# Performance work log

Hardware: AMD Instinct MI355X
Metric: run time of the kernel (lower is better)

The kernel has to match this reference:

```python
import jax, jax.numpy as jnp
import numpy as np

N_NODES = 50000
N_EDGES = 800000
IN_FEATS = 128
NUM_HEADS = 4
OUT_FEATS = 16
NEG_SLOPE = 0.2


def setup_inputs() -> dict:
    key = jax.random.key(0)
    k_feat, k_src, k_dst, k_w, k_al, k_ar = jax.random.split(key, 6)
    feat = jax.random.normal(k_feat, (N_NODES, IN_FEATS), dtype=jnp.float32)
    src = jax.random.randint(k_src, (N_EDGES,), 0, N_NODES, dtype=jnp.int32)
    # guarantee every destination node has in-degree >= 1 (segment softmax well-defined)
    dst_rand = jax.random.randint(k_dst, (N_EDGES - N_NODES,), 0, N_NODES, dtype=jnp.int32)
    dst = jnp.concatenate([jnp.arange(N_NODES, dtype=jnp.int32), dst_rand])
    # xavier-normal-ish parameter scales
    W = jax.random.normal(k_w, (IN_FEATS, NUM_HEADS * OUT_FEATS), dtype=jnp.float32) * (
        1.414 * (2.0 / (IN_FEATS + NUM_HEADS * OUT_FEATS)) ** 0.5)
    attn_l = jax.random.normal(k_al, (NUM_HEADS, OUT_FEATS), dtype=jnp.float32) * 0.1
    attn_r = jax.random.normal(k_ar, (NUM_HEADS, OUT_FEATS), dtype=jnp.float32) * 0.1
    bias = jnp.zeros((NUM_HEADS * OUT_FEATS,), dtype=jnp.float32)
    return {"feat": feat, "src": src, "dst": dst, "W": W,
            "attn_l": attn_l, "attn_r": attn_r, "bias": bias}


def reference(feat, src, dst, W, attn_l, attn_r, bias):
    N = feat.shape[0]
    H, D = attn_l.shape
    # shared projection (homogeneous-graph branch, eval mode: dropout = identity)
    ft = (feat @ W).reshape(N, H, D)                      # [N,H,D]
    el = jnp.einsum('nhd,hd->nh', ft, attn_l)             # [N,H]
    er = jnp.einsum('nhd,hd->nh', ft, attn_r)             # [N,H]
    # u_add_v + leaky_relu -> per-edge logits [E,H]
    e = jax.nn.leaky_relu(el[src] + er[dst], negative_slope=NEG_SLOPE)
    # edge_softmax: stable segment softmax over destination neighborhoods
    m = jax.ops.segment_max(e, dst, num_segments=N)       # [N,H]
    ex = jnp.exp(e - m[dst])                              # [E,H]
    s = jax.ops.segment_sum(ex, dst, num_segments=N)      # [N,H]
    a = ex / s[dst]                                       # [E,H]
    # u_mul_e + sum: gather src features, weight, scatter-add to dst
    msg = ft[src] * a[:, :, None]                         # [E,H,D]
    rst = jax.ops.segment_sum(msg, dst, num_segments=N)   # [N,H,D]
    return rst + bias.reshape(1, H, D)
```

## Files before the change

kernel.cpp:

```cpp
#include <hip/hip_runtime.h>
#include <hip/hip_fp16.h>
#include <math.h>

#define IN_FEATS 128
#define HD 64
#define H 4
#define D 16
#define SLAB 64
#define NXCD 8
#define FILL_EPT 8
#define FILL_CHUNK (256 * FILL_EPT)

typedef __attribute__((ext_vector_type(8))) short bf16x8;
typedef __attribute__((ext_vector_type(4))) float f32x4;

__device__ __forceinline__ short f2bf(float x) {
    unsigned u = __float_as_uint(x);
    u += 0x7FFFu + ((u >> 16) & 1u);
    return (short)(u >> 16);
}

__global__ __launch_bounds__(256) void k_proj(
    const float* __restrict__ feat, const float* __restrict__ W,
    const float* __restrict__ attn_l, const float* __restrict__ attn_r,
    __half* __restrict__ ft16, float* __restrict__ el, float* __restrict__ er,
    int* __restrict__ cnt, int N)
{
    const int tid   = threadIdx.x;
    const int wid   = tid >> 6;
    const int lane  = tid & 63;
    const int nbase = (blockIdx.x * 4 + wid) * 16;
    if (nbase >= N) return;

    if (lane < 16 && nbase + lane < N) cnt[nbase + lane] = 0;

    const int m = lane & 15;
    const int g = lane >> 4;
    const int arow = min(nbase + m, N - 1);

    bf16x8 afrag[4];
    const float* ap = feat + (size_t)arow * IN_FEATS + 8 * g;
    #pragma unroll
    for (int s = 0; s < 4; ++s) {
        float4 lo = *(const float4*)(ap + 32 * s);
        float4 hi = *(const float4*)(ap + 32 * s + 4);
        bf16x8 a;
        a[0] = f2bf(lo.x); a[1] = f2bf(lo.y); a[2] = f2bf(lo.z); a[3] = f2bf(lo.w);
        a[4] = f2bf(hi.x); a[5] = f2bf(hi.y); a[6] = f2bf(hi.z); a[7] = f2bf(hi.w);
        afrag[s] = a;
    }

    f32x4 acc[4] = {{0.f,0.f,0.f,0.f}, {0.f,0.f,0.f,0.f},
                    {0.f,0.f,0.f,0.f}, {0.f,0.f,0.f,0.f}};
    #pragma unroll
    for (int s = 0; s < 4; ++s) {
        const float* wp = W + (size_t)(32 * s + 8 * g) * HD + m;
        #pragma unroll
        for (int c4 = 0; c4 < 4; ++c4) {
            const float* bp = wp + 16 * c4;
            bf16x8 b;
            #pragma unroll
            for (int j = 0; j < 8; ++j) b[j] = f2bf(bp[(size_t)j * HD]);
            acc[c4] = __builtin_amdgcn_mfma_f32_16x16x32_bf16(
                          afrag[s], b, acc[c4], 0, 0, 0);
        }
    }

    #pragma unroll
    for (int c4 = 0; c4 < 4; ++c4) {
        const float al = attn_l[c4 * 16 + m];
        const float ar = attn_r[c4 * 16 + m];
        #pragma unroll
        for (int r = 0; r < 4; ++r) {
            const int node = nbase + 4 * g + r;
            float v = acc[c4][r];
            if (node < N)
                ft16[(size_t)node * HD + c4 * 16 + m] = __float2half(v);
            float l = v * al, rr = v * ar;
            #pragma unroll
            for (int off = 8; off >= 1; off >>= 1) {
                l  += __shfl_xor(l,  off, 16);
                rr += __shfl_xor(rr, off, 16);
            }
            if (m == 0 && node < N) {
                el[node * H + c4] = l;
                er[node * H + c4] = rr;
            }
        }
    }
}

__global__ __launch_bounds__(256) void k_fill(
    const int* __restrict__ src, const int* __restrict__ dst,
    int* __restrict__ cnt, unsigned short* __restrict__ slab, int E, int R)
{
    const int xcd   = blockIdx.x & (NXCD - 1);
    const int chunk = blockIdx.x >> 3;
    const int dlo   = xcd * R;
    const int base  = chunk * FILL_CHUNK + threadIdx.x * FILL_EPT;

    if (base + FILL_EPT <= E) {
        int4 d0 = *(const int4*)(dst + base);
        int4 d1 = *(const int4*)(dst + base + 4);
        int4 s0 = *(const int4*)(src + base);
        int4 s1 = *(const int4*)(src + base + 4);
        int dd[FILL_EPT] = {d0.x, d0.y, d0.z, d0.w, d1.x, d1.y, d1.z, d1.w};
        int ss[FILL_EPT] = {s0.x, s0.y, s0.z, s0.w, s1.x, s1.y, s1.z, s1.w};
        #pragma unroll
        for (int i = 0; i < FILL_EPT; ++i) {
            int d = dd[i];
            if ((unsigned)(d - dlo) < (unsigned)R) {
                int p = atomicAdd(&cnt[d], 1);
                if (p < SLAB) slab[(size_t)d * SLAB + p] = (unsigned short)ss[i];
            }
        }
    } else {
        for (int e = base; e < E; ++e) {
            int d = dst[e];
            if ((unsigned)(d - dlo) < (unsigned)R) {
                int p = atomicAdd(&cnt[d], 1);
                if (p < SLAB) slab[(size_t)d * SLAB + p] = (unsigned short)src[e];
            }
        }
    }
}

__global__ __launch_bounds__(256) void k_aggregate(
    const __half* __restrict__ ft16, const float* __restrict__ el,
    const float* __restrict__ er, const int* __restrict__ cnt,
    const unsigned short* __restrict__ slab, const float* __restrict__ bias,
    float* __restrict__ out, int N, int R)
{
    const int tid = threadIdx.x;
    const int xcd = blockIdx.x & (NXCD - 1);
    const int loc = blockIdx.x >> 3;
    const int ln  = loc * 4 + (tid >> 6);
    if (ln >= R) return;
    const int n = xcd * R + ln;
    if (n >= N) return;

    const int lane = tid & 63;
    const int h    = lane >> 4;

    const float ern = er[n * H + h];
    const int deg = min(cnt[n], SLAB);
    const unsigned short* __restrict__ row = slab + (size_t)n * SLAB;

    float acc  = 0.f;
    float ssum = 0.f;

    for (int j = 0; j < deg; j += 8) {
        int4 a = *(const int4*)(row + j);

        int s0 = a.x & 0xFFFF;
        int s1 = (j + 1 < deg) ? ((a.x >> 16) & 0xFFFF) : s0;
        int s2 = (j + 2 < deg) ? (a.y & 0xFFFF)         : s0;
        int s3 = (j + 3 < deg) ? ((a.y >> 16) & 0xFFFF) : s0;
        int s4 = (j + 4 < deg) ? (a.z & 0xFFFF)         : s0;
        int s5 = (j + 5 < deg) ? ((a.z >> 16) & 0xFFFF) : s0;
        int s6 = (j + 6 < deg) ? (a.w & 0xFFFF)         : s0;
        int s7 = (j + 7 < deg) ? ((a.w >> 16) & 0xFFFF) : s0;

        float e0 = el[s0 * H + h];
        float e1 = el[s1 * H + h];
        float e2 = el[s2 * H + h];
        float e3 = el[s3 * H + h];
        float e4 = el[s4 * H + h];
        float e5 = el[s5 * H + h];
        float e6 = el[s6 * H + h];
        float e7 = el[s7 * H + h];

        float f0 = __half2float(ft16[(size_t)s0 * HD + lane]);
        float f1 = __half2float(ft16[(size_t)s1 * HD + lane]);
        float f2 = __half2float(ft16[(size_t)s2 * HD + lane]);
        float f3 = __half2float(ft16[(size_t)s3 * HD + lane]);
        float f4 = __half2float(ft16[(size_t)s4 * HD + lane]);
        float f5 = __half2float(ft16[(size_t)s5 * HD + lane]);
        float f6 = __half2float(ft16[(size_t)s6 * HD + lane]);
        float f7 = __half2float(ft16[(size_t)s7 * HD + lane]);

        e0 += ern; e0 = (e0 > 0.f) ? e0 : 0.2f * e0;
        e1 += ern; e1 = (e1 > 0.f) ? e1 : 0.2f * e1;
        e2 += ern; e2 = (e2 > 0.f) ? e2 : 0.2f * e2;
        e3 += ern; e3 = (e3 > 0.f) ? e3 : 0.2f * e3;
        e4 += ern; e4 = (e4 > 0.f) ? e4 : 0.2f * e4;
        e5 += ern; e5 = (e5 > 0.f) ? e5 : 0.2f * e5;
        e6 += ern; e6 = (e6 > 0.f) ? e6 : 0.2f * e6;
        e7 += ern; e7 = (e7 > 0.f) ? e7 : 0.2f * e7;

        float x0 = __expf(e0);
        float x1 = (j + 1 < deg) ? __expf(e1) : 0.f;
        float x2 = (j + 2 < deg) ? __expf(e2) : 0.f;
        float x3 = (j + 3 < deg) ? __expf(e3) : 0.f;
        float x4 = (j + 4 < deg) ? __expf(e4) : 0.f;
        float x5 = (j + 5 < deg) ? __expf(e5) : 0.f;
        float x6 = (j + 6 < deg) ? __expf(e6) : 0.f;
        float x7 = (j + 7 < deg) ? __expf(e7) : 0.f;

        ssum += ((x0 + x1) + (x2 + x3)) + ((x4 + x5) + (x6 + x7));
        acc = fmaf(x0, f0, acc);
        acc = fmaf(x1, f1, acc);
        acc = fmaf(x2, f2, acc);
        acc = fmaf(x3, f3, acc);
        acc = fmaf(x4, f4, acc);
        acc = fmaf(x5, f5, acc);
        acc = fmaf(x6, f6, acc);
        acc = fmaf(x7, f7, acc);
    }

    out[(size_t)n * HD + lane] = acc / ssum + bias[lane];
}

extern "C" void kernel_launch(void* const* d_in, const int* in_sizes, int n_in,
                              void* d_out, int out_size, void* d_ws, size_t ws_size,
                              hipStream_t stream)
{
    const float* feat   = (const float*)d_in[0];
    const int*   src    = (const int*)  d_in[1];
    const int*   dst    = (const int*)  d_in[2];
    const float* W      = (const float*)d_in[3];
    const float* attn_l = (const float*)d_in[4];
    const float* attn_r = (const float*)d_in[5];
    const float* bias   = (const float*)d_in[6];
    float*       out    = (float*)d_out;

    const int N = in_sizes[0] / IN_FEATS;
    const int E = in_sizes[1];
    const int R = (N + NXCD - 1) / NXCD;

    char* ws = (char*)d_ws;
    __half*         ft16 = (__half*)ws;         ws += (size_t)N * HD * sizeof(__half);
    float*          el   = (float*)ws;          ws += (size_t)N * H * sizeof(float);
    float*          er   = (float*)ws;          ws += (size_t)N * H * sizeof(float);
    int*            cnt  = (int*)ws;            ws += (size_t)N * sizeof(int);
    unsigned short* slab = (unsigned short*)ws;

    const int ntiles  = (N + 15) / 16;
    const int nchunks = (E + FILL_CHUNK - 1) / FILL_CHUNK;
    k_proj<<<(ntiles + 3) / 4, 256, 0, stream>>>(feat, W, attn_l, attn_r,
                                                 ft16, el, er, cnt, N);
    k_fill<<<nchunks * NXCD, 256, 0, stream>>>(src, dst, cnt, slab, E, R);
    k_aggregate<<<((R + 3) / 4) * NXCD, 256, 0, stream>>>(ft16, el, er, cnt,
                                                          slab, bias, out, N, R);
}
```

Baseline: 88.92 us.

## Pre-bin edges by XCD partition before atomic slab fill

Replaces the single fill kernel with two passes. Previously every XCD's blocks read all edges and filtered out the ones for their own destination range. Now one pass reads each edge once and uses wave ballots to bucket packed (src, local dst) words into per-wave, per-XCD segments. A second pass has each XCD's blocks read only their own buckets and do the count atomics and slab writes locally. The goal is to drop the 8x redundant edge reads while keeping atomics XCD-local, at the cost of an extra kernel launch, a scratch buffer and overflow atomics that can run on a remote XCD.

```diff
diff --git a/kernel.cpp b/kernel.cpp
--- a/kernel.cpp
+++ b/kernel.cpp
@@ -8,8 +8,8 @@
 #define D 16
 #define SLAB 64
 #define NXCD 8
-#define FILL_EPT 8
-#define FILL_CHUNK (256 * FILL_EPT)
+#define BIN_EPW 256
+#define BCAP 96
 
 typedef __attribute__((ext_vector_type(8))) short bf16x8;
 typedef __attribute__((ext_vector_type(4))) float f32x4;
@@ -90,37 +90,92 @@
     }
 }
 
-__global__ __launch_bounds__(256) void k_fill(
+__global__ __launch_bounds__(256) void k_bin3(
     const int* __restrict__ src, const int* __restrict__ dst,
-    int* __restrict__ cnt, unsigned short* __restrict__ slab, int E, int R)
-{
-    const int xcd   = blockIdx.x & (NXCD - 1);
-    const int chunk = blockIdx.x >> 3;
-    const int dlo   = xcd * R;
-    const int base  = chunk * FILL_CHUNK + threadIdx.x * FILL_EPT;
-
-    if (base + FILL_EPT <= E) {
-        int4 d0 = *(const int4*)(dst + base);
-        int4 d1 = *(const int4*)(dst + base + 4);
-        int4 s0 = *(const int4*)(src + base);
-        int4 s1 = *(const int4*)(src + base + 4);
-        int dd[FILL_EPT] = {d0.x, d0.y, d0.z, d0.w, d1.x, d1.y, d1.z, d1.w};
-        int ss[FILL_EPT] = {s0.x, s0.y, s0.z, s0.w, s1.x, s1.y, s1.z, s1.w};
+    unsigned int* __restrict__ seg, int* __restrict__ wcnt,
+    int* __restrict__ cnt, unsigned short* __restrict__ slab,
+    int E, int R, int nwaves)
+{
+    const int tid  = threadIdx.x;
+    const int lane = tid & 63;
+    const int w    = (blockIdx.x * 256 + tid) >> 6;
+    if (w >= nwaves) return;
+
+    const unsigned long long lmask = (1ull << lane) - 1ull;
+    const int base = w * BIN_EPW;
+    int cl0 = 0, cl1 = 0, cl2 = 0, cl3 = 0, cl4 = 0, cl5 = 0, cl6 = 0, cl7 = 0;
+    unsigned int* myseg = seg + (size_t)w * 8 * BCAP;
+
+    #pragma unroll
+    for (int b4 = 0; b4 < BIN_EPW; b4 += 64) {
+        const int e = base + b4 + lane;
+        const bool valid = (e < E);
+        const int d  = valid ? dst[e] : 0;
+        const int s  = valid ? src[e] : 0;
+        const int bk = valid ? (int)((unsigned)d / (unsigned)R) : -1;
+        const unsigned int pl = (unsigned int)(s & 0xFFFF)
+                              | ((unsigned int)(d - bk * R) << 16);
+
         #pragma unroll
-        for (int i = 0; i < FILL_EPT; ++i) {
-            int d = dd[i];
-            if ((unsigned)(d - dlo) < (unsigned)R) {
-                int p = atomicAdd(&cnt[d], 1);
-                if (p < SLAB) slab[(size_t)d * SLAB + p] = (unsigned short)ss[i];
+        for (int b = 0; b < 8; ++b) {
+            unsigned long long mask = __ballot(bk == b);
+            int cl = (b == 0) ? cl0 : (b == 1) ? cl1 : (b == 2) ? cl2 :
+                     (b == 3) ? cl3 : (b == 4) ? cl4 : (b == 5) ? cl5 :
+                     (b == 6) ? cl6 : cl7;
+            if (mask) {
+                if (bk == b) {
+                    int idx = cl + __popcll(mask & lmask);
+                    if (idx < BCAP) {
+                        myseg[b * BCAP + idx] = pl;
+                    } else {
+                        int pos = atomicAdd(&cnt[d], 1);
+                        if (pos < SLAB)
+                            slab[(size_t)d * SLAB + pos] = (unsigned short)s;
+                    }
+                }
+                cl += __popcll(mask);
+                if      (b == 0) cl0 = cl;
+                else if (b == 1) cl1 = cl;
+                else if (b == 2) cl2 = cl;
+                else if (b == 3) cl3 = cl;
+                else if (b == 4) cl4 = cl;
+                else if (b == 5) cl5 = cl;
+                else if (b == 6) cl6 = cl;
+                else             cl7 = cl;
             }
         }
-    } else {
-        for (int e = base; e < E; ++e) {
-            int d = dst[e];
-            if ((unsigned)(d - dlo) < (unsigned)R) {
-                int p = atomicAdd(&cnt[d], 1);
-                if (p < SLAB) slab[(size_t)d * SLAB + p] = (unsigned short)src[e];
-            }
+    }
+
+    if (lane == 0) {
+        int* wc = wcnt + w * 8;
+        wc[0] = min(cl0, BCAP); wc[1] = min(cl1, BCAP);
+        wc[2] = min(cl2, BCAP); wc[3] = min(cl3, BCAP);
+        wc[4] = min(cl4, BCAP); wc[5] = min(cl5, BCAP);
+        wc[6] = min(cl6, BCAP); wc[7] = min(cl7, BCAP);
+    }
+}
+
+__global__ __launch_bounds__(256) void k_fill3(
+    const unsigned int* __restrict__ seg, const int* __restrict__ wcnt,
+    int* __restrict__ cnt, unsigned short* __restrict__ slab,
+    int R, int nwaves)
+{
+    const int tid    = threadIdx.x;
+    const int xcd    = blockIdx.x & (NXCD - 1);
+    const int slot   = blockIdx.x >> 3;
+    const int nslots = gridDim.x >> 3;
+    const int wid    = tid >> 6;
+    const int lane   = tid & 63;
+    const int dlo    = xcd * R;
+
+    for (int w = slot * 4 + wid; w < nwaves; w += nslots * 4) {
+        const int c = wcnt[w * 8 + xcd];
+        const unsigned int* p = seg + ((size_t)w * 8 + xcd) * BCAP;
+        for (int i = lane; i < c; i += 64) {
+            unsigned int pl = p[i];
+            int d = dlo + (int)(pl >> 16);
+            int pos = atomicAdd(&cnt[d], 1);
+            if (pos < SLAB) slab[(size_t)d * SLAB + pos] = (unsigned short)(pl & 0xFFFF);
         }
     }
 }
@@ -227,19 +282,23 @@
     const int N = in_sizes[0] / IN_FEATS;
     const int E = in_sizes[1];
     const int R = (N + NXCD - 1) / NXCD;
+    const int nwaves = (E + BIN_EPW - 1) / BIN_EPW;
 
     char* ws = (char*)d_ws;
     __half*         ft16 = (__half*)ws;         ws += (size_t)N * HD * sizeof(__half);
     float*          el   = (float*)ws;          ws += (size_t)N * H * sizeof(float);
     float*          er   = (float*)ws;          ws += (size_t)N * H * sizeof(float);
     int*            cnt  = (int*)ws;            ws += (size_t)N * sizeof(int);
-    unsigned short* slab = (unsigned short*)ws;
-
-    const int ntiles  = (N + 15) / 16;
-    const int nchunks = (E + FILL_CHUNK - 1) / FILL_CHUNK;
+    unsigned short* slab = (unsigned short*)ws; ws += (size_t)N * SLAB * sizeof(unsigned short);
+    int*            wcnt = (int*)ws;            ws += (size_t)nwaves * 8 * sizeof(int);
+    unsigned int*   seg  = (unsigned int*)ws;
+
+    const int ntiles = (N + 15) / 16;
     k_proj<<<(ntiles + 3) / 4, 256, 0, stream>>>(feat, W, attn_l, attn_r,
                                                  ft16, el, er, cnt, N);
-    k_fill<<<nchunks * NXCD, 256, 0, stream>>>(src, dst, cnt, slab, E, R);
+    k_bin3<<<(nwaves + 3) / 4, 256, 0, stream>>>(src, dst, seg, wcnt,
+                                                 cnt, slab, E, R, nwaves);
+    k_fill3<<<128 * NXCD, 256, 0, stream>>>(seg, wcnt, cnt, slab, R, nwaves);
     k_aggregate<<<((R + 3) / 4) * NXCD, 256, 0, stream>>>(ft16, el, er, cnt,
                                                           slab, bias, out, N, R);
 }
```

Measured after the change: 91.38 us. 1.03x slower.
